# Optimization experiments

Hardware: AMD Instinct MI355X
Metric: run time of the kernel (lower is better)

## Reference

```python
import jax, jax.numpy as jnp
import numpy as np

T, D, F, E, K = 2048, 1024, 4096, 8, 2


def setup_inputs() -> dict:
    key = jax.random.key(0)
    ks = jax.random.split(key, 4)
    return {
        "x": jax.random.normal(ks[0], (T, D), dtype=jnp.float32),
        "Wg": jax.random.normal(ks[1], (D, E), dtype=jnp.float32) * (1.0 / np.sqrt(D)),
        "bg": jnp.zeros((E,), dtype=jnp.float32),
        "W1": jax.random.normal(ks[2], (E, D, F), dtype=jnp.float32) * (1.0 / np.sqrt(D)),
        "b1": jnp.zeros((E, F), dtype=jnp.float32),
        "W2": jax.random.normal(ks[3], (E, F, D), dtype=jnp.float32) * (1.0 / np.sqrt(F)),
        "b2": jnp.zeros((E, D), dtype=jnp.float32),
        "top_k": K,
    }


def reference(x, Wg, bg, W1, b1, W2, b2, top_k):
    num_tokens, d_model = x.shape
    n_experts = W1.shape[0]

    # Gate + baseline top-k routing: router returns top-k softmax probs.
    gate_logits = x @ Wg + bg                       # [T, E]
    gate_probs_all = jax.nn.softmax(gate_logits, axis=-1)
    top_k_probs, top_k_indices = jax.lax.top_k(gate_probs_all, top_k)  # [T, K]

    # Load-balancing aux loss (top-1 token counts x mean gate prob).
    top1 = top_k_indices[:, 0]
    tokens_per_expert = jnp.zeros((n_experts,), x.dtype).at[top1].add(1.0)
    aux_loss = jnp.sum(tokens_per_expert / (num_tokens + 1e-8)
                       * gate_probs_all.mean(axis=0)) * n_experts

    # Combine weights: scatter top-k probs into dense [T, E]; zero elsewhere,
    # so the dense per-expert compute below reproduces the sparse dispatch math.
    comb = jnp.zeros((num_tokens, n_experts), x.dtype)
    comb = comb.at[jnp.arange(num_tokens)[:, None], top_k_indices].add(top_k_probs)

    # Expert FFNs (linear_fc1 -> relu -> linear_fc2), batched over experts.
    h = jax.nn.relu(jnp.einsum('td,edf->etf', x, W1) + b1[:, None, :])  # [E, T, F]
    y = jnp.einsum('etf,efd->etd', h, W2) + b2[:, None, :]              # [E, T, D]

    # Weighted scatter-combine.
    output = jnp.einsum('etd,te->td', y, comb)                          # [T, D]
    return output, aux_loss
```

## Files before the change

kernel.cpp:

```cpp
#include <hip/hip_runtime.h>
#include <stdint.h>

#define T_TOK 2048
#define DMODEL 1024
#define FDIM 4096
#define NEXP 8
#define CAP 2048

typedef __attribute__((ext_vector_type(8))) short short8;
typedef __attribute__((ext_vector_type(4))) float f32x4;
typedef __attribute__((ext_vector_type(4))) unsigned short us4;
typedef __attribute__((ext_vector_type(8))) unsigned short us8;

__device__ __forceinline__ unsigned short f2bf(float f) {
  union { float f; unsigned int u; } v; v.f = f;
  unsigned int r = (v.u + 0x7fffu + ((v.u >> 16) & 1u)) >> 16;
  return (unsigned short)r;
}

__device__ __forceinline__ void async16(const unsigned short* g, unsigned short* l) {
  __builtin_amdgcn_global_load_lds(
      (const __attribute__((address_space(1))) unsigned int*)g,
      (__attribute__((address_space(3))) unsigned int*)l,
      16, 0, 0);
}

__global__ void gate_kernel(const float* __restrict__ x, const float* __restrict__ Wg,
                            const float* __restrict__ bg,
                            int* cnt, int* top1cnt, float* sumprob,
                            int* list, float* wlist, int* tok2slot) {
  int wave = threadIdx.x >> 6;
  int lane = threadIdx.x & 63;
  __shared__ float sprob[8];
  __shared__ int   stop1[8];
  __shared__ int   ent_e[32];
  __shared__ float ent_p[32];
  if (threadIdx.x < 8) { sprob[threadIdx.x] = 0.f; stop1[threadIdx.x] = 0; }
  __syncthreads();

#pragma unroll
  for (int i = 0; i < 4; i++) {
    int s = wave * 4 + i;
    int t = blockIdx.x * 16 + s;
    float acc[8];
#pragma unroll
    for (int e = 0; e < 8; e++) acc[e] = 0.f;
    const float* xr = x + (size_t)t * DMODEL;
    for (int c = lane; c < DMODEL / 4; c += 64) {
      f32x4 xv = ((const f32x4*)xr)[c];
      const float* wr = Wg + (size_t)c * 4 * 8;
#pragma unroll
      for (int q = 0; q < 4; q++)
#pragma unroll
        for (int e = 0; e < 8; e++) acc[e] += xv[q] * wr[q * 8 + e];
    }
#pragma unroll
    for (int off = 32; off > 0; off >>= 1) {
#pragma unroll
      for (int e = 0; e < 8; e++) acc[e] += __shfl_down(acc[e], off);
    }
    if (lane == 0) {
      float p[8];
      float m = -1e30f;
#pragma unroll
      for (int e = 0; e < 8; e++) { p[e] = acc[e] + bg[e]; m = fmaxf(m, p[e]); }
      float sum = 0.f;
#pragma unroll
      for (int e = 0; e < 8; e++) { p[e] = __expf(p[e] - m); sum += p[e]; }
      float inv = 1.f / sum;
#pragma unroll
      for (int e = 0; e < 8; e++) p[e] *= inv;
      int e1 = 0; float p1 = p[0];
#pragma unroll
      for (int e = 1; e < 8; e++) if (p[e] > p1) { p1 = p[e]; e1 = e; }
      int e2 = -1; float p2 = -1.f;
#pragma unroll
      for (int e = 0; e < 8; e++) if (e != e1 && p[e] > p2) { p2 = p[e]; e2 = e; }
      atomicAdd(&stop1[e1], 1);
#pragma unroll
      for (int e = 0; e < 8; e++) atomicAdd(&sprob[e], p[e]);
      ent_e[2 * s]     = e1; ent_p[2 * s]     = p1;
      ent_e[2 * s + 1] = e2; ent_p[2 * s + 1] = p2;
    }
  }
  __syncthreads();

  if (threadIdx.x < 8) {
    int e = threadIdx.x;
    int n = 0;
#pragma unroll
    for (int j = 0; j < 32; j++) n += (ent_e[j] == e) ? 1 : 0;
    if (n) {
      int pos = atomicAdd(cnt + e, n);
#pragma unroll
      for (int j = 0; j < 32; j++) {
        if (ent_e[j] == e) {
          int t = blockIdx.x * 16 + (j >> 1);
          list[e * CAP + pos]  = t;
          wlist[e * CAP + pos] = ent_p[j];
          tok2slot[2 * t + (j & 1)] = (e << 16) | pos;
          pos++;
        }
      }
    }
    atomicAdd(sumprob + e, sprob[e]);
    int c = stop1[e];
    if (c) atomicAdd(top1cnt + e, c);
  }
}

__global__ void offs_aux_kernel(const int* cnt, const int* top1cnt, const float* sumprob,
                                int* offs, float* out_aux) {
  if (threadIdx.x == 0 && blockIdx.x == 0) {
    int off = 0;
    float aux = 0.f;
    for (int e = 0; e < 8; e++) {
      offs[e] = off; off += cnt[e];
      aux += ((float)top1cnt[e] / ((float)T_TOK + 1e-8f)) * (sumprob[e] / (float)T_TOK);
    }
    *out_aux = aux * (float)NEXP;
  }
}

__global__ void gather_kernel(const float* __restrict__ x, const int* __restrict__ list,
                              const int* __restrict__ cnt, const int* __restrict__ offs,
                              unsigned short* __restrict__ xg) {
  int e = blockIdx.x >> 11;
  int i = blockIdx.x & 2047;
  if (i >= cnt[e]) return;
  int t = list[e * CAP + i];
  int row = offs[e] + i;
  const f32x4* src = (const f32x4*)(x + (size_t)t * DMODEL);
  us4* dst = (us4*)(xg + (size_t)row * DMODEL);
  int j = threadIdx.x;
  f32x4 v = src[j];
  us4 o; o.x = f2bf(v.x); o.y = f2bf(v.y); o.z = f2bf(v.z); o.w = f2bf(v.w);
  dst[j] = o;
}

__launch_bounds__(256)
__global__ void convt_kernel(const float* __restrict__ in, unsigned short* __restrict__ out,
                             int Kfull, int Nfull, int KS, int k_off, int NS, int n_off) {
  int e = blockIdx.y;
  int ntn = NS >> 6;
  int tk = blockIdx.x / ntn, tn = blockIdx.x % ntn;
  const float* src = in + (size_t)e * Kfull * Nfull + (size_t)(k_off + tk * 64) * Nfull + n_off + tn * 64;
  unsigned short* dst = out + (size_t)e * NS * KS + (size_t)(tn * 64) * KS + tk * 64;
  __shared__ unsigned short Ls[64 * 72];
  int t = threadIdx.x;
  int k = t >> 4, n4 = (t & 15) * 4;
#pragma unroll
  for (int i = 0; i < 4; i++) {
    int kk = k + 16 * i;
    f32x4 v = *(const f32x4*)&src[(size_t)kk * Nfull + n4];
    Ls[(n4 + 0) * 72 + kk] = f2bf(v.x);
    Ls[(n4 + 1) * 72 + kk] = f2bf(v.y);
    Ls[(n4 + 2) * 72 + kk] = f2bf(v.z);
    Ls[(n4 + 3) * 72 + kk] = f2bf(v.w);
  }
  __syncthreads();
  int n = t >> 3, k8 = (t & 7) * 8;
#pragma unroll
  for (int j = 0; j < 2; j++) {
    int nn = n + 32 * j;
    us8 v = *(const us8*)&Ls[nn * 72 + k8];
    *(us8*)&dst[(size_t)nn * KS + k8] = v;
  }
}

__launch_bounds__(256)
__global__ void gemm1_kernel(const unsigned short* __restrict__ xg,
                             const unsigned short* __restrict__ Wt,
                             const float* __restrict__ b1,
                             const int* __restrict__ cnt, const int* __restrict__ offs,
                             unsigned short* __restrict__ h, int NS, int n_off) {
  int e = blockIdx.x;
  int mt = blockIdx.z;
  int count = cnt[e];
  if (mt * 128 >= count) return;
  int nloc = blockIdx.y * 128;
  int base = offs[e];
  const unsigned short* A = xg + (size_t)(base + mt * 128) * DMODEL;
  const unsigned short* B = Wt + (size_t)e * NS * DMODEL + (size_t)nloc * DMODEL;

  __shared__ unsigned short As[4 * 128 * 8];
  __shared__ unsigned short Bs[4 * 128 * 8];

  int tid = threadIdx.x;
  int w = tid >> 6, lane = tid & 63;
  int wr = w >> 1, wc = w & 1;
  int l16 = lane & 15, quad = lane >> 4;

  f32x4 acc[4][4];
#pragma unroll
  for (int i = 0; i < 4; i++)
#pragma unroll
    for (int j = 0; j < 4; j++)
#pragma unroll
      for (int r = 0; r < 4; r++) acc[i][j][r] = 0.f;

  const unsigned short* Aw0 = A + (size_t)lane * DMODEL + w * 8;
  const unsigned short* Aw1 = A + (size_t)(64 + lane) * DMODEL + w * 8;
  const unsigned short* Bw0 = B + (size_t)lane * DMODEL + w * 8;
  const unsigned short* Bw1 = B + (size_t)(64 + lane) * DMODEL + w * 8;
  unsigned short* AsW0 = &As[w * 1024];
  unsigned short* AsW1 = &As[w * 1024 + 512];
  unsigned short* BsW0 = &Bs[w * 1024];
  unsigned short* BsW1 = &Bs[w * 1024 + 512];

  for (int kb = 0; kb < DMODEL / 32; kb++) {
    int ko = kb * 32;
    async16(Aw0 + ko, AsW0);
    async16(Aw1 + ko, AsW1);
    async16(Bw0 + ko, BsW0);
    async16(Bw1 + ko, BsW1);
    __syncthreads();
    short8 af[4], bf[4];
#pragma unroll
    for (int i = 0; i < 4; i++)
      af[i] = *(const short8*)&As[quad * 1024 + (wr * 64 + i * 16 + l16) * 8];
#pragma unroll
    for (int j = 0; j < 4; j++)
      bf[j] = *(const short8*)&Bs[quad * 1024 + (wc * 64 + j * 16 + l16) * 8];
#pragma unroll
    for (int i = 0; i < 4; i++)
#pragma unroll
      for (int j = 0; j < 4; j++)
        acc[i][j] = __builtin_amdgcn_mfma_f32_16x16x32_bf16(af[i], bf[j], acc[i][j], 0, 0, 0);
    __syncthreads();
  }

#pragma unroll
  for (int j = 0; j < 4; j++) {
    int ncl = nloc + wc * 64 + j * 16 + l16;
    float bias = b1[e * FDIM + n_off + ncl];
#pragma unroll
    for (int i = 0; i < 4; i++) {
      int rbase = mt * 128 + wr * 64 + i * 16 + quad * 4;
#pragma unroll
      for (int r = 0; r < 4; r++) {
        int row = rbase + r;
        if (row < count) {
          float v = fmaxf(acc[i][j][r] + bias, 0.f);
          h[(size_t)(base + row) * NS + ncl] = f2bf(v);
        }
      }
    }
  }
}

__launch_bounds__(256)
__global__ void gemm2_kernel(const unsigned short* __restrict__ h,
                             const unsigned short* __restrict__ Wt,
                             const float* __restrict__ b2,
                             const int* __restrict__ cnt, const int* __restrict__ offs,
                             float* __restrict__ y, int KS, int first) {
  int e = blockIdx.x;
  int mt = blockIdx.z;
  int count = cnt[e];
  if (mt * 128 >= count) return;
  int nloc = blockIdx.y * 128;
  int base = offs[e];
  const unsigned short* A = h + (size_t)(base + mt * 128) * KS;
  const unsigned short* B = Wt + (size_t)e * DMODEL * KS + (size_t)nloc * KS;

  __shared__ unsigned short As[4 * 128 * 8];
  __shared__ unsigned short Bs[4 * 128 * 8];

  int tid = threadIdx.x;
  int w = tid >> 6, lane = tid & 63;
  int wr = w >> 1, wc = w & 1;
  int l16 = lane & 15, quad = lane >> 4;

  f32x4 acc[4][4];
#pragma unroll
  for (int i = 0; i < 4; i++)
#pragma unroll
    for (int j = 0; j < 4; j++)
#pragma unroll
      for (int r = 0; r < 4; r++) acc[i][j][r] = 0.f;

  const unsigned short* Aw0 = A + (size_t)lane * KS + w * 8;
  const unsigned short* Aw1 = A + (size_t)(64 + lane) * KS + w * 8;
  const unsigned short* Bw0 = B + (size_t)lane * KS + w * 8;
  const unsigned short* Bw1 = B + (size_t)(64 + lane) * KS + w * 8;
  unsigned short* AsW0 = &As[w * 1024];
  unsigned short* AsW1 = &As[w * 1024 + 512];
  unsigned short* BsW0 = &Bs[w * 1024];
  unsigned short* BsW1 = &Bs[w * 1024 + 512];

  for (int kb = 0; kb < KS / 32; kb++) {
    int ko = kb * 32;
    async16(Aw0 + ko, AsW0);
    async16(Aw1 + ko, AsW1);
    async16(Bw0 + ko, BsW0);
    async16(Bw1 + ko, BsW1);
    __syncthreads();
    short8 af[4], bf[4];
#pragma unroll
    for (int i = 0; i < 4; i++)
      af[i] = *(const short8*)&As[quad * 1024 + (wr * 64 + i * 16 + l16) * 8];
#pragma unroll
    for (int j = 0; j < 4; j++)
      bf[j] = *(const short8*)&Bs[quad * 1024 + (wc * 64 + j * 16 + l16) * 8];
#pragma unroll
    for (int i = 0; i < 4; i++)
#pragma unroll
      for (int j = 0; j < 4; j++)
        acc[i][j] = __builtin_amdgcn_mfma_f32_16x16x32_bf16(af[i], bf[j], acc[i][j], 0, 0, 0);
    __syncthreads();
  }

  float bv[4];
#pragma unroll
  for (int j = 0; j < 4; j++)
    bv[j] = first ? b2[e * DMODEL + nloc + wc * 64 + j * 16 + l16] : 0.f;

#pragma unroll
  for (int i = 0; i < 4; i++) {
    int rbase = mt * 128 + wr * 64 + i * 16 + quad * 4;
#pragma unroll
    for (int r = 0; r < 4; r++) {
      int row = rbase + r;
      if (row >= count) continue;
      float* yr = y + (size_t)(base + row) * DMODEL;
#pragma unroll
      for (int j = 0; j < 4; j++) {
        int ncol = nloc + wc * 64 + j * 16 + l16;
        float v = acc[i][j][r] + bv[j];
        if (first) yr[ncol] = v;
        else       yr[ncol] += v;
      }
    }
  }
}

__global__ void combine_kernel(const float* __restrict__ y, const int* __restrict__ offs,
                               const int* __restrict__ tok2slot, const float* __restrict__ wlist,
                               float* __restrict__ out) {
  int t = blockIdx.x;
  int s0 = tok2slot[2 * t], s1 = tok2slot[2 * t + 1];
  int e0 = s0 >> 16, p0 = s0 & 0xffff;
  int e1 = s1 >> 16, p1 = s1 & 0xffff;
  float w0 = wlist[e0 * CAP + p0], w1 = wlist[e1 * CAP + p1];
  int r0 = offs[e0] + p0, r1 = offs[e1] + p1;
  int j = threadIdx.x * 4;
  f32x4 a = *(const f32x4*)&y[(size_t)r0 * DMODEL + j];
  f32x4 b = *(const f32x4*)&y[(size_t)r1 * DMODEL + j];
  f32x4 o;
  o.x = w0 * a.x + w1 * b.x;
  o.y = w0 * a.y + w1 * b.y;
  o.z = w0 * a.z + w1 * b.z;
  o.w = w0 * a.w + w1 * b.w;
  *(f32x4*)&out[(size_t)t * DMODEL + j] = o;
}

extern "C" void kernel_launch(void* const* d_in, const int* in_sizes, int n_in,
                              void* d_out, int out_size, void* d_ws, size_t ws_size,
                              hipStream_t stream) {
  const float* x  = (const float*)d_in[0];
  const float* Wg = (const float*)d_in[1];
  const float* bg = (const float*)d_in[2];
  const float* W1 = (const float*)d_in[3];
  const float* b1 = (const float*)d_in[4];
  const float* W2 = (const float*)d_in[5];
  const float* b2 = (const float*)d_in[6];
  float* out = (float*)d_out;

  char* ws = (char*)d_ws;
  int*   cnt      = (int*)(ws + 0);
  int*   top1cnt  = (int*)(ws + 32);
  int*   offs     = (int*)(ws + 64);
  float* sumprob  = (float*)(ws + 96);
  int*   list     = (int*)(ws + 4096);
  float* wlist    = (float*)(ws + 69632);
  int*   tok2slot = (int*)(ws + 135168);
  unsigned short* xg = (unsigned short*)(ws + 151552);

  const size_t fixed = 8540160ull + 16777216ull;
  int S = 8;
  if      (ws_size >= fixed + 100663296ull)     S = 1;
  else if (ws_size >= fixed + 100663296ull / 2) S = 2;
  else if (ws_size >= fixed + 100663296ull / 4) S = 4;
  const int NS1 = FDIM / S;
  unsigned short* h  = (unsigned short*)(ws + 8540160);
  float*          y  = (float*)(ws + 8540160 + 33554432ull / S);
  unsigned short* Wt = (unsigned short*)(ws + 8540160 + 33554432ull / S + 16777216ull);

  hipMemsetAsync(ws, 0, 1024, stream);

  gate_kernel<<<T_TOK / 16, 256, 0, stream>>>(x, Wg, bg, cnt, top1cnt, sumprob, list, wlist, tok2slot);
  offs_aux_kernel<<<1, 64, 0, stream>>>(cnt, top1cnt, sumprob, offs, out + (size_t)T_TOK * DMODEL);
  gather_kernel<<<NEXP * CAP, 256, 0, stream>>>(x, list, cnt, offs, xg);

  for (int s = 0; s < S; s++) {
    convt_kernel<<<dim3((DMODEL / 64) * (NS1 / 64), NEXP), 256, 0, stream>>>(
        W1, Wt, DMODEL, FDIM, DMODEL, 0, NS1, s * NS1);
    gemm1_kernel<<<dim3(NEXP, NS1 / 128, 16), 256, 0, stream>>>(
        xg, Wt, b1, cnt, offs, h, NS1, s * NS1);
    convt_kernel<<<dim3((NS1 / 64) * (DMODEL / 64), NEXP), 256, 0, stream>>>(
        W2, Wt, FDIM, DMODEL, NS1, s * NS1, DMODEL, 0);
    gemm2_kernel<<<dim3(NEXP, DMODEL / 128, 16), 256, 0, stream>>>(
        h, Wt, b2, cnt, offs, y, NS1, s == 0 ? 1 : 0);
  }

  combine_kernel<<<T_TOK, 256, 0, stream>>>(y, offs, tok2slot, wlist, out);
}
```

Before: 591.4 us.

## Double-buffer LDS tiles with 64-wide K steps in both expert GEMMs

Result: slower. 607.2 us (+2.7%).

```diff
diff --git a/kernel.cpp b/kernel.cpp
--- a/kernel.cpp
+++ b/kernel.cpp
@@ -23,6 +23,19 @@
       (const __attribute__((address_space(1))) unsigned int*)g,
       (__attribute__((address_space(3))) unsigned int*)l,
       16, 0, 0);
+}
+
+__device__ __forceinline__ void stage64(const unsigned short* Ar0, const unsigned short* Ar1,
+                                        const unsigned short* Br0, const unsigned short* Br1,
+                                        int ko, unsigned short* Ab, unsigned short* Bb) {
+  async16(Ar0 + ko,     Ab);
+  async16(Ar1 + ko,     Ab + 512);
+  async16(Ar0 + ko + 8, Ab + 1024);
+  async16(Ar1 + ko + 8, Ab + 1536);
+  async16(Br0 + ko,     Bb);
+  async16(Br1 + ko,     Bb + 512);
+  async16(Br0 + ko + 8, Bb + 1024);
+  async16(Br1 + ko + 8, Bb + 1536);
 }
 
 __global__ void gate_kernel(const float* __restrict__ x, const float* __restrict__ Wg,
@@ -183,8 +196,8 @@
   const unsigned short* A = xg + (size_t)(base + mt * 128) * DMODEL;
   const unsigned short* B = Wt + (size_t)e * NS * DMODEL + (size_t)nloc * DMODEL;
 
-  __shared__ unsigned short As[4 * 128 * 8];
-  __shared__ unsigned short Bs[4 * 128 * 8];
+  __shared__ unsigned short As[2 * 8 * 128 * 8];
+  __shared__ unsigned short Bs[2 * 8 * 128 * 8];
 
   int tid = threadIdx.x;
   int w = tid >> 6, lane = tid & 63;
@@ -199,35 +212,45 @@
 #pragma unroll
       for (int r = 0; r < 4; r++) acc[i][j][r] = 0.f;
 
-  const unsigned short* Aw0 = A + (size_t)lane * DMODEL + w * 8;
-  const unsigned short* Aw1 = A + (size_t)(64 + lane) * DMODEL + w * 8;
-  const unsigned short* Bw0 = B + (size_t)lane * DMODEL + w * 8;
-  const unsigned short* Bw1 = B + (size_t)(64 + lane) * DMODEL + w * 8;
-  unsigned short* AsW0 = &As[w * 1024];
-  unsigned short* AsW1 = &As[w * 1024 + 512];
-  unsigned short* BsW0 = &Bs[w * 1024];
-  unsigned short* BsW1 = &Bs[w * 1024 + 512];
-
-  for (int kb = 0; kb < DMODEL / 32; kb++) {
-    int ko = kb * 32;
-    async16(Aw0 + ko, AsW0);
-    async16(Aw1 + ko, AsW1);
-    async16(Bw0 + ko, BsW0);
-    async16(Bw1 + ko, BsW1);
+  const unsigned short* Ar0 = A + (size_t)lane * DMODEL + w * 16;
+  const unsigned short* Ar1 = A + (size_t)(64 + lane) * DMODEL + w * 16;
+  const unsigned short* Br0 = B + (size_t)lane * DMODEL + w * 16;
+  const unsigned short* Br1 = B + (size_t)(64 + lane) * DMODEL + w * 16;
+
+  stage64(Ar0, Ar1, Br0, Br1, 0, &As[w * 2048], &Bs[w * 2048]);
+  __syncthreads();
+
+  int cb = 0;
+  const int KT = DMODEL / 64;
+  for (int kt = 0; kt < KT; kt++) {
+    if (kt + 1 < KT)
+      stage64(Ar0, Ar1, Br0, Br1, (kt + 1) * 64,
+              &As[(cb ^ 1) * 8192 + w * 2048], &Bs[(cb ^ 1) * 8192 + w * 2048]);
+    const unsigned short* Ac = &As[cb * 8192 + quad * 1024];
+    const unsigned short* Bc = &Bs[cb * 8192 + quad * 1024];
+    short8 a0[4], a1[4], b0[4], b1v[4];
+#pragma unroll
+    for (int i = 0; i < 4; i++) {
+      a0[i]  = *(const short8*)&Ac[(wr * 64 + i * 16 + l16) * 8];
+      a1[i]  = *(const short8*)&Ac[4096 + (wr * 64 + i * 16 + l16) * 8];
+    }
+#pragma unroll
+    for (int j = 0; j < 4; j++) {
+      b0[j]  = *(const short8*)&Bc[(wc * 64 + j * 16 + l16) * 8];
+      b1v[j] = *(const short8*)&Bc[4096 + (wc * 64 + j * 16 + l16) * 8];
+    }
+#pragma unroll
+    for (int i = 0; i < 4; i++)
+#pragma unroll
+      for (int j = 0; j < 4; j++)
+        acc[i][j] = __builtin_amdgcn_mfma_f32_16x16x32_bf16(a0[i], b0[j], acc[i][j], 0, 0, 0);
+#pragma unroll
+    for (int i = 0; i < 4; i++)
+#pragma unroll
+      for (int j = 0; j < 4; j++)
+        acc[i][j] = __builtin_amdgcn_mfma_f32_16x16x32_bf16(a1[i], b1v[j], acc[i][j], 0, 0, 0);
     __syncthreads();
-    short8 af[4], bf[4];
-#pragma unroll
-    for (int i = 0; i < 4; i++)
-      af[i] = *(const short8*)&As[quad * 1024 + (wr * 64 + i * 16 + l16) * 8];
-#pragma unroll
-    for (int j = 0; j < 4; j++)
-      bf[j] = *(const short8*)&Bs[quad * 1024 + (wc * 64 + j * 16 + l16) * 8];
-#pragma unroll
-    for (int i = 0; i < 4; i++)
-#pragma unroll
-      for (int j = 0; j < 4; j++)
-        acc[i][j] = __builtin_amdgcn_mfma_f32_16x16x32_bf16(af[i], bf[j], acc[i][j], 0, 0, 0);
-    __syncthreads();
+    cb ^= 1;
   }
 
 #pragma unroll
@@ -264,8 +287,8 @@
   const unsigned short* A = h + (size_t)(base + mt * 128) * KS;
   const unsigned short* B = Wt + (size_t)e * DMODEL * KS + (size_t)nloc * KS;
 
-  __shared__ unsigned short As[4 * 128 * 8];
-  __shared__ unsigned short Bs[4 * 128 * 8];
+  __shared__ unsigned short As[2 * 8 * 128 * 8];
+  __shared__ unsigned short Bs[2 * 8 * 128 * 8];
 
   int tid = threadIdx.x;
   int w = tid >> 6, lane = tid & 63;
@@ -280,35 +303,45 @@
 #pragma unroll
       for (int r = 0; r < 4; r++) acc[i][j][r] = 0.f;
 
-  const unsigned short* Aw0 = A + (size_t)lane * KS + w * 8;
-  const unsigned short* Aw1 = A + (size_t)(64 + lane) * KS + w * 8;
-  const unsigned short* Bw0 = B + (size_t)lane * KS + w * 8;
-  const unsigned short* Bw1 = B + (size_t)(64 + lane) * KS + w * 8;
-  unsigned short* AsW0 = &As[w * 1024];
-  unsigned short* AsW1 = &As[w * 1024 + 512];
-  unsigned short* BsW0 = &Bs[w * 1024];
-  unsigned short* BsW1 = &Bs[w * 1024 + 512];
-
-  for (int kb = 0; kb < KS / 32; kb++) {
-    int ko = kb * 32;
-    async16(Aw0 + ko, AsW0);
-    async16(Aw1 + ko, AsW1);
-    async16(Bw0 + ko, BsW0);
-    async16(Bw1 + ko, BsW1);
+  const unsigned short* Ar0 = A + (size_t)lane * KS + w * 16;
+  const unsigned short* Ar1 = A + (size_t)(64 + lane) * KS + w * 16;
+  const unsigned short* Br0 = B + (size_t)lane * KS + w * 16;
+  const unsigned short* Br1 = B + (size_t)(64 + lane) * KS + w * 16;
+
+  stage64(Ar0, Ar1, Br0, Br1, 0, &As[w * 2048], &Bs[w * 2048]);
+  __syncthreads();
+
+  int cb = 0;
+  const int KT = KS / 64;
+  for (int kt = 0; kt < KT; kt++) {
+    if (kt + 1 < KT)
+      stage64(Ar0, Ar1, Br0, Br1, (kt + 1) * 64,
+              &As[(cb ^ 1) * 8192 + w * 2048], &Bs[(cb ^ 1) * 8192 + w * 2048]);
+    const unsigned short* Ac = &As[cb * 8192 + quad * 1024];
+    const unsigned short* Bc = &Bs[cb * 8192 + quad * 1024];
+    short8 a0[4], a1[4], b0[4], b1v[4];
+#pragma unroll
+    for (int i = 0; i < 4; i++) {
+      a0[i]  = *(const short8*)&Ac[(wr * 64 + i * 16 + l16) * 8];
+      a1[i]  = *(const short8*)&Ac[4096 + (wr * 64 + i * 16 + l16) * 8];
+    }
+#pragma unroll
+    for (int j = 0; j < 4; j++) {
+      b0[j]  = *(const short8*)&Bc[(wc * 64 + j * 16 + l16) * 8];
+      b1v[j] = *(const short8*)&Bc[4096 + (wc * 64 + j * 16 + l16) * 8];
+    }
+#pragma unroll
+    for (int i = 0; i < 4; i++)
+#pragma unroll
+      for (int j = 0; j < 4; j++)
+        acc[i][j] = __builtin_amdgcn_mfma_f32_16x16x32_bf16(a0[i], b0[j], acc[i][j], 0, 0, 0);
+#pragma unroll
+    for (int i = 0; i < 4; i++)
+#pragma unroll
+      for (int j = 0; j < 4; j++)
+        acc[i][j] = __builtin_amdgcn_mfma_f32_16x16x32_bf16(a1[i], b1v[j], acc[i][j], 0, 0, 0);
     __syncthreads();
-    short8 af[4], bf[4];
-#pragma unroll
-    for (int i = 0; i < 4; i++)
-      af[i] = *(const short8*)&As[quad * 1024 + (wr * 64 + i * 16 + l16) * 8];
-#pragma unroll
-    for (int j = 0; j < 4; j++)
-      bf[j] = *(const short8*)&Bs[quad * 1024 + (wc * 64 + j * 16 + l16) * 8];
-#pragma unroll
-    for (int i = 0; i < 4; i++)
-#pragma unroll
-      for (int j = 0; j < 4; j++)
-        acc[i][j] = __builtin_amdgcn_mfma_f32_16x16x32_bf16(af[i], bf[j], acc[i][j], 0, 0, 0);
-    __syncthreads();
+    cb ^= 1;
   }
 
   float bv[4];
```
